# Kernel tuning notes

Hardware: AMD Instinct MI355X
Metric: run time of the kernel (lower is better)

The kernel has to match this reference:

```python
import jax, jax.numpy as jnp
import numpy as np

EMBED_DIM = 96
OUT_DIM = 192
HEADS = 2
HEAD_DIM = OUT_DIM // HEADS  # 96
STRIDE_Q = (1, 2, 2)
STRIDE_KV = (1, 8, 8)
SCALE = 1.0 / float(np.sqrt(HEAD_DIM))


def layer_norm(x, g, b, eps=1e-5):
    m = jnp.mean(x, -1, keepdims=True)
    v = jnp.mean(jnp.square(x - m), -1, keepdims=True)
    return (x - m) * jax.lax.rsqrt(v + eps) * g + b


def pool(x, thw, conv_w, g, b, stride):
    # x: [B, heads, N, d] with cls token at position 0; depthwise conv3d pool + LayerNorm(d)
    B, nh, N, d = x.shape
    T, H, W = thw
    cls_tok, rest = x[:, :, :1], x[:, :, 1:]
    rest = rest.transpose(0, 1, 3, 2).reshape(B * nh, d, T, H, W)
    rest = jax.lax.conv_general_dilated(
        rest, conv_w, stride, [(1, 1), (1, 1), (1, 1)],
        dimension_numbers=('NCDHW', 'OIDHW', 'NCDHW'), feature_group_count=d)
    T2, H2, W2 = rest.shape[2], rest.shape[3], rest.shape[4]
    rest = rest.reshape(B, nh, d, -1).transpose(0, 1, 3, 2)
    x = jnp.concatenate([cls_tok, rest], axis=2)
    return layer_norm(x, g, b), (T2, H2, W2)


def rel_idx(q_n, k_n):
    # decomposed relative-distance indices with q/k resolution ratio scaling
    q_r = max(k_n / q_n, 1.0)
    k_r = max(q_n / k_n, 1.0)
    d = (jnp.arange(q_n, dtype=jnp.float32)[:, None] * q_r
         - jnp.arange(k_n, dtype=jnp.float32)[None, :] * k_r + (k_n - 1) * k_r)
    return d.astype(jnp.int32)


def add_rel_pos(attn, q, q_thw, k_thw, rph, rpw, rpt):
    qt, qh, qw = q_thw
    kt, kh, kw = k_thw
    Rh = rph[rel_idx(qh, kh)]  # [qh, kh, d]
    Rw = rpw[rel_idx(qw, kw)]  # [qw, kw, d]
    Rt = rpt[rel_idx(qt, kt)]  # [qt, kt, d]
    B, nh, qN, d = q.shape
    r_q = q[:, :, 1:].reshape(B, nh, qt, qh, qw, d)
    rel_h = jnp.einsum('bythwc,hkc->bythwk', r_q, Rh)  # k = kh
    rel_w = jnp.einsum('bythwc,wkc->bythwk', r_q, Rw)  # k = kw
    rel_t = jnp.einsum('bythwc,tkc->bythwk', r_q, Rt)  # k = kt
    rel = (rel_t[..., :, None, None] + rel_h[..., None, :, None]
           + rel_w[..., None, None, :]).reshape(B, nh, qt * qh * qw, kt * kh * kw)
    return attn.at[:, :, 1:, 1:].add(rel)


def _forward(x, qkv_w, qkv_b, proj_w, proj_b, pq_w, nq_g, nq_b, pk_w, nk_g, nk_b,
             pv_w, nv_g, nv_b, rel_pos_h, rel_pos_w, rel_pos_t, thw):
    B, N, C = x.shape
    qkv = (x @ qkv_w.T + qkv_b).reshape(B, N, 3, HEADS, HEAD_DIM).transpose(2, 0, 3, 1, 4)
    q, k, v = qkv[0], qkv[1], qkv[2]  # each [B, heads, N, head_dim]
    k, k_thw = pool(k, thw, pk_w, nk_g, nk_b, STRIDE_KV)
    v, _ = pool(v, thw, pv_w, nv_g, nv_b, STRIDE_KV)
    q, q_thw = pool(q, thw, pq_w, nq_g, nq_b, STRIDE_Q)
    attn = jnp.einsum('bhqd,bhkd->bhqk', q * SCALE, k)
    attn = add_rel_pos(attn, q, q_thw, k_thw, rel_pos_h, rel_pos_w, rel_pos_t)
    attn = jax.nn.softmax(attn, axis=-1)
    out = jnp.einsum('bhqk,bhkd->bhqd', attn, v) + q  # residual_pool, with cls embed
    out = out.transpose(0, 2, 1, 3).reshape(B, -1, OUT_DIM)
    return out @ proj_w.T + proj_b


def setup_inputs() -> dict:
    key = jax.random.key(0)
    ks = jax.random.split(key, 10)
    T, H, W = 8, 56, 56
    N = 1 + T * H * W  # 25089
    B = 4
    std = 0.02
    return {
        'x': jax.random.normal(ks[0], (B, N, EMBED_DIM), jnp.float32),
        'qkv_w': jax.random.normal(ks[1], (3 * OUT_DIM, EMBED_DIM), jnp.float32) * std,
        'qkv_b': jnp.zeros((3 * OUT_DIM,), jnp.float32),
        'proj_w': jax.random.normal(ks[2], (OUT_DIM, OUT_DIM), jnp.float32) * std,
        'proj_b': jnp.zeros((OUT_DIM,), jnp.float32),
        'pq_w': jax.random.normal(ks[3], (HEAD_DIM, 1, 3, 3, 3), jnp.float32) * std,
        'nq_g': jnp.ones((HEAD_DIM,), jnp.float32),
        'nq_b': jnp.zeros((HEAD_DIM,), jnp.float32),
        'pk_w': jax.random.normal(ks[4], (HEAD_DIM, 1, 3, 3, 3), jnp.float32) * std,
        'nk_g': jnp.ones((HEAD_DIM,), jnp.float32),
        'nk_b': jnp.zeros((HEAD_DIM,), jnp.float32),
        'pv_w': jax.random.normal(ks[5], (HEAD_DIM, 1, 3, 3, 3), jnp.float32) * std,
        'nv_g': jnp.ones((HEAD_DIM,), jnp.float32),
        'nv_b': jnp.zeros((HEAD_DIM,), jnp.float32),
        'rel_pos_h': jax.random.normal(ks[6], (55, HEAD_DIM), jnp.float32) * std,
        'rel_pos_w': jax.random.normal(ks[7], (55, HEAD_DIM), jnp.float32) * std,
        'rel_pos_t': jax.random.normal(ks[8], (15, HEAD_DIM), jnp.float32) * std,
        'thw_t': 8, 'thw_h': 56, 'thw_w': 56,
    }


def reference(x, qkv_w, qkv_b, proj_w, proj_b, pq_w, nq_g, nq_b, pk_w, nk_g, nk_b,
              pv_w, nv_g, nv_b, rel_pos_h, rel_pos_w, rel_pos_t, thw_t, thw_h, thw_w):
    thw = (int(thw_t), int(thw_h), int(thw_w))
    return _forward(x, qkv_w, qkv_b, proj_w, proj_b, pq_w, nq_g, nq_b, pk_w, nk_g, nk_b,
                    pv_w, nv_g, nv_b, rel_pos_h, rel_pos_w, rel_pos_t, thw)
```

## Files before the change

kernel.cpp:

```cpp
#include <hip/hip_runtime.h>
#include <hip/hip_bf16.h>

typedef short short8 __attribute__((ext_vector_type(8)));
typedef float floatx4 __attribute__((ext_vector_type(4)));
typedef float floatx4v __attribute__((ext_vector_type(4)));

#define SCALE_F 0.10206207261596575f

static __device__ __forceinline__ float b2f(unsigned short u){
  unsigned int v = ((unsigned int)u) << 16; float f;
  __builtin_memcpy(&f, &v, 4); return f;
}
static __device__ __forceinline__ unsigned short f2b(float f){
  __hip_bfloat16 h = __float2bfloat16(f);
  unsigned short u; __builtin_memcpy(&u, &h, 2); return u;
}
static __device__ __forceinline__ int map20(int i){
  return (i < 2) ? i : 7 + ((i-2)/3)*8 + ((i-2)%3);
}

struct ConvDesc {
  const void* src[17];
  long long off[17];
  int count[17];
};

__global__ __launch_bounds__(256) void k_convert(ConvDesc d, unsigned short* dst_base,
                                                 int* flagp, const unsigned int* xprobe)
{
  __shared__ int sflag;
  if (threadIdx.x < 64){
    unsigned int w = xprobe[1024 + threadIdx.x];
    int e = (w >> 7) & 0xFF;
    int pl = (e >= 90 && e <= 140) ? 1 : 0;
    unsigned long long m = __ballot(pl);
    if (threadIdx.x == 0){
      sflag = (__popcll(m) < 40) ? 1 : 0;
      if (blockIdx.x == 0 && blockIdx.y == 0) *flagp = sflag;
    }
  }
  __syncthreads();
  const int flag = sflag;
  const int t = blockIdx.y + 1;
  const int cnt = d.count[t];
  unsigned short* dst = dst_base + d.off[t];
  const float* sf = (const float*)d.src[t];
  const unsigned short* su = (const unsigned short*)d.src[t];
  for (int i = blockIdx.x*blockDim.x + threadIdx.x; i < cnt; i += gridDim.x*blockDim.x){
    dst[i] = flag ? f2b(sf[i]) : su[i];
  }
}

static __device__ __forceinline__ void load_x_frag(
    const void* xr_, int flag, size_t elem_off, short8& a0, short8& a1, short8& a2)
{
  if (flag){
    const float* xr = (const float*)xr_ + elem_off;
    floatx4v f0 = *(const floatx4v*)(xr),      f1 = *(const floatx4v*)(xr+4);
    floatx4v f2 = *(const floatx4v*)(xr+32),   f3 = *(const floatx4v*)(xr+36);
    floatx4v f4 = *(const floatx4v*)(xr+64),   f5 = *(const floatx4v*)(xr+68);
    #pragma unroll
    for (int j = 0; j < 4; ++j){
      a0[j] = (short)f2b(f0[j]); a0[j+4] = (short)f2b(f1[j]);
      a1[j] = (short)f2b(f2[j]); a1[j+4] = (short)f2b(f3[j]);
      a2[j] = (short)f2b(f4[j]); a2[j+4] = (short)f2b(f5[j]);
    }
  } else {
    const unsigned short* xr = (const unsigned short*)xr_ + elem_off;
    a0 = *(const short8*)(xr);
    a1 = *(const short8*)(xr + 32);
    a2 = *(const short8*)(xr + 64);
  }
}

__global__ __launch_bounds__(256) void k_qkv_q(
    const void* __restrict__ x, const unsigned short* __restrict__ w,
    const unsigned short* __restrict__ bias, unsigned short* __restrict__ qr,
    const int* __restrict__ flagp)
{
  const int flag = *flagp;
  const int lane = threadIdx.x & 63;
  const int wv = threadIdx.x >> 6;
  const int kq = (lane >> 4) * 8;
  const int m_base = blockIdx.x * 64 + wv * 16;

  int ma = m_base + (lane & 15); if (ma > 100355) ma = 100355;
  short8 a0, a1, a2;
  load_x_frag(x, flag, (size_t)ma*96 + kq, a0, a1, a2);

  size_t base0[4];
  int mrow[4];
  #pragma unroll
  for (int r = 0; r < 4; ++r){
    int m = m_base + (lane >> 4)*4 + r;
    mrow[r] = m;
    int bb = m / 25089; int n = m - bb*25089;
    base0[r] = ((size_t)(bb*2)*25089 + n)*96;
  }

  #pragma unroll
  for (int ct = 0; ct < 12; ++ct){
    int col = ct*16 + (lane & 15);
    const unsigned short* wrow = w + col*96 + kq;
    short8 b0 = *(const short8*)(wrow);
    short8 b1 = *(const short8*)(wrow + 32);
    short8 b2 = *(const short8*)(wrow + 64);
    float bv = b2f(bias[col]);
    floatx4 acc = {0.f,0.f,0.f,0.f};
    acc = __builtin_amdgcn_mfma_f32_16x16x32_bf16(a0, b0, acc, 0,0,0);
    acc = __builtin_amdgcn_mfma_f32_16x16x32_bf16(a1, b1, acc, 0,0,0);
    acc = __builtin_amdgcn_mfma_f32_16x16x32_bf16(a2, b2, acc, 0,0,0);
    const int head = ct / 6;
    const int dstat = (ct % 6) * 16;
    size_t hoff = (size_t)head * 2408544 + dstat + (lane & 15);
    #pragma unroll
    for (int r = 0; r < 4; ++r){
      if (mrow[r] < 100356) qr[base0[r] + hoff] = f2b(acc[r] + bv);
    }
  }
}

__global__ __launch_bounds__(256) void k_qkv_kv(
    const void* __restrict__ x, const unsigned short* __restrict__ w,
    const unsigned short* __restrict__ bias,
    unsigned short* __restrict__ kc, unsigned short* __restrict__ vc,
    unsigned short* __restrict__ kcls, unsigned short* __restrict__ vcls,
    const int* __restrict__ flagp)
{
  const int flag = *flagp;
  const int isv = blockIdx.y;
  const int lane = threadIdx.x & 63;
  const int wv = threadIdx.x >> 6;
  const int kq = (lane >> 4) * 8;
  const int quad = lane >> 4;
  const int col_l = lane & 15;
  const int rbase = blockIdx.x * 64 + wv * 16;

  int rhoA = rbase + col_l; if (rhoA > 12803) rhoA = 12803;
  int bA, nA;
  if (rhoA < 4){ bA = rhoA; nA = 0; }
  else {
    int rp = rhoA - 4;
    bA = rp / 3200; int rem = rp - bA*3200;
    int t = rem / 400; int s = rem - t*400;
    int ry = s / 20, rx = s - ry*20;
    nA = 1 + (t*56 + map20(ry))*56 + map20(rx);
  }
  short8 a0, a1, a2;
  load_x_frag(x, flag, ((size_t)bA*25089 + nA)*96 + kq, a0, a1, a2);

  int isCls[4], bI[4], baseI[4], valid[4];
  #pragma unroll
  for (int r = 0; r < 4; ++r){
    int rho = rbase + quad*4 + r;
    valid[r] = (rho < 12804);
    if (rho > 12803) rho = 12803;
    if (rho < 4){ isCls[r] = 1; bI[r] = rho; baseI[r] = 0; }
    else {
      int rp = rho - 4;
      int b = rp / 3200; int rem = rp - b*3200;
      int t = rem / 400; int s = rem - t*400;
      int ry = s / 20, rx = s - ry*20;
      isCls[r] = 0; bI[r] = b;
      baseI[r] = (((b*8 + t)*20 + ry)*20 + rx)*192;
    }
  }

  unsigned short* buf  = isv ? vc : kc;
  unsigned short* bufc = isv ? vcls : kcls;
  #pragma unroll
  for (int ct = 0; ct < 12; ++ct){
    const int col = 192 + (isv*12 + ct)*16 + col_l;
    const unsigned short* wrow = w + col*96 + kq;
    short8 b0 = *(const short8*)(wrow);
    short8 b1 = *(const short8*)(wrow + 32);
    short8 b2 = *(const short8*)(wrow + 64);
    float bv = b2f(bias[col]);
    floatx4 acc = {0.f,0.f,0.f,0.f};
    acc = __builtin_amdgcn_mfma_f32_16x16x32_bf16(a0, b0, acc, 0,0,0);
    acc = __builtin_amdgcn_mfma_f32_16x16x32_bf16(a1, b1, acc, 0,0,0);
    acc = __builtin_amdgcn_mfma_f32_16x16x32_bf16(a2, b2, acc, 0,0,0);
    const int head = ct / 6;
    const int dstat = (ct % 6) * 16;
    #pragma unroll
    for (int r = 0; r < 4; ++r){
      if (valid[r]){
        float o = acc[r] + bv;
        if (isCls[r]) bufc[(bI[r]*2 + head)*96 + dstat + col_l] = f2b(o);
        else          buf[baseI[r] + head*96 + dstat + col_l]   = f2b(o);
      }
    }
  }
}

__global__ __launch_bounds__(384) void k_poolq(
    const unsigned short* __restrict__ qr, const unsigned short* __restrict__ cw,
    const unsigned short* __restrict__ g, const unsigned short* __restrict__ bta,
    unsigned short* __restrict__ qp)
{
  __shared__ float wlds[27*96];
  __shared__ float gls[96], bls[96];
  __shared__ float ls1[29*12], ls2[29*12];
  __shared__ float lmean[29], linvs[29];

  const int y  = blockIdx.x;
  const int t  = blockIdx.y;
  const int bh = blockIdx.z;
  const int tid = threadIdx.x;
  const bool has_cls = (y == 0 && t == 0);
  const unsigned short* base = qr + (size_t)bh*2408544;

  for (int idx = tid; idx < 27*96; idx += 384){
    int tap = idx / 96, d = idx - tap*96;
    wlds[idx] = b2f(cw[d*27 + tap]);
  }
  for (int idx = tid; idx < 96; idx += 384){
    gls[idx] = b2f(g[idx]); bls[idx] = b2f(bta[idx]);
  }
  __syncthreads();

  const int x = tid / 12, dg = tid - x*12;
  float val[8] = {0,0,0,0,0,0,0,0};

  if (x < 28){
    #pragma unroll
    for (int dt = 0; dt < 3; ++dt){
      int tt = t + dt - 1; if (tt < 0 || tt >= 8) continue;
      #pragma unroll
      for (int dy = 0; dy < 3; ++dy){
        int yy = 2*y + dy - 1; if (yy < 0 || yy >= 56) continue;
        #pragma unroll
        for (int dx = 0; dx < 3; ++dx){
          int xv = 2*x + dx - 1; if (xv < 0 || xv >= 56) continue;
          const int tap = (dt*3+dy)*3+dx;
          short8 v = *(const short8*)(base + (size_t)(1 + (tt*56 + yy)*56 + xv)*96 + dg*8);
          const float* wr = wlds + tap*96 + dg*8;
          #pragma unroll
          for (int j = 0; j < 8; ++j) val[j] += b2f((unsigned short)v[j]) * wr[j];
        }
      }
    }
    float s1 = 0.f, s2 = 0.f;
    #pragma unroll
    for (int j = 0; j < 8; ++j){ s1 += val[j]; s2 += val[j]*val[j]; }
    ls1[x*12+dg] = s1; ls2[x*12+dg] = s2;
  } else if (has_cls && tid >= 348 && tid < 360){
    int cdg = tid - 348;
    short8 v = *(const short8*)(base + cdg*8);
    float s1 = 0.f, s2 = 0.f;
    #pragma unroll
    for (int j = 0; j < 8; ++j){ val[j] = b2f((unsigned short)v[j]); s1 += val[j]; s2 += val[j]*val[j]; }
    ls1[28*12+cdg] = s1; ls2[28*12+cdg] = s2;
  }
  __syncthreads();

  if (tid < 28 || (tid == 28 && has_cls)){
    float s1 = 0.f, s2 = 0.f;
    #pragma unroll
    for (int k = 0; k < 12; ++k){ s1 += ls1[tid*12+k]; s2 += ls2[tid*12+k]; }
    float mean = s1 * (1.f/96.f);
    float var  = s2 * (1.f/96.f) - mean*mean;
    lmean[tid] = mean; linvs[tid] = rsqrtf(var + 1e-5f);
  }
  __syncthreads();

  if (x < 28){
    float mean = lmean[x], inv = linvs[x];
    int tok = 1 + (t*28 + y)*28 + x;
    short8 o;
    #pragma unroll
    for (int j = 0; j < 8; ++j)
      o[j] = (short)f2b((val[j] - mean)*inv*gls[dg*8+j] + bls[dg*8+j]);
    *(short8*)(qp + ((size_t)bh*6273 + tok)*96 + dg*8) = o;
  } else if (has_cls && tid >= 348 && tid < 360){
    int cdg = tid - 348;
    float mean = lmean[28], inv = linvs[28];
    short8 o;
    #pragma unroll
    for (int j = 0; j < 8; ++j)
      o[j] = (short)f2b((val[j] - mean)*inv*gls[cdg*8+j] + bls[cdg*8+j]);
    *(short8*)(qp + (size_t)bh*6273*96 + cdg*8) = o;
  }
}

__global__ __launch_bounds__(128) void k_poolkv(
    const unsigned short* __restrict__ kc, const unsigned short* __restrict__ vc,
    const unsigned short* __restrict__ kcls, const unsigned short* __restrict__ vcls,
    const unsigned short* __restrict__ cwk, const unsigned short* __restrict__ gk, const unsigned short* __restrict__ bk,
    const unsigned short* __restrict__ cwv, const unsigned short* __restrict__ gv, const unsigned short* __restrict__ bv,
    unsigned short* __restrict__ kp, unsigned short* __restrict__ vt)
{
  const int bid = blockIdx.x;
  const int isv = blockIdx.y;
  const int bh = bid / 416; const int key = bid - bh*416;
  const int d = threadIdx.x;
  if (key >= 393){
    if (d < 96){
      if (isv == 0) kp[((size_t)bh*416 + key)*96 + d] = 0;
      else          vt[((size_t)bh*96 + d)*416 + key] = 0;
    }
    return;
  }
  const int b = bh >> 1, head = bh & 1;
  const unsigned short* buf  = isv ? vc : kc;
  const unsigned short* bufc = isv ? vcls : kcls;
  const unsigned short* cw = (isv == 0) ? cwk : cwv;
  const unsigned short* g  = (isv == 0) ? gk : gv;
  const unsigned short* bt = (isv == 0) ? bk : bv;
  float val = 0.f;
  if (d < 96){
    if (key == 0) val = b2f(bufc[bh*96 + d]);
    else {
      int s = key - 1; int t = s / 49; int r2 = s - t*49; int y = r2 / 7; int xx = r2 - y*7;
      const unsigned short* wr = cw + d*27;
      float sum = 0.f;
      #pragma unroll
      for (int dt = 0; dt < 3; ++dt){
        int tt = t + dt - 1; if (tt < 0 || tt >= 8) continue;
        #pragma unroll
        for (int dy = 0; dy < 3; ++dy){
          if (y == 0 && dy == 0) continue;
          int ry = (y == 0) ? (dy - 1) : 2 + 3*(y-1) + dy;
          #pragma unroll
          for (int dx = 0; dx < 3; ++dx){
            if (xx == 0 && dx == 0) continue;
            int rx = (xx == 0) ? (dx - 1) : 2 + 3*(xx-1) + dx;
            sum += b2f(buf[(((b*8 + tt)*20 + ry)*20 + rx)*192 + head*96 + d]) * b2f(wr[(dt*3+dy)*3+dx]);
          }
        }
      }
      val = sum;
    }
  }
  __shared__ float r1[128], r2s[128];
  r1[threadIdx.x] = (d < 96) ? val : 0.f;
  r2s[threadIdx.x] = (d < 96) ? val*val : 0.f;
  __syncthreads();
  for (int off = 64; off > 0; off >>= 1){
    if ((int)threadIdx.x < off){ r1[threadIdx.x] += r1[threadIdx.x+off]; r2s[threadIdx.x] += r2s[threadIdx.x+off]; }
    __syncthreads();
  }
  if (d < 96){
    float mean = r1[0] * (1.f/96.f);
    float var  = r2s[0] * (1.f/96.f) - mean*mean;
    float inv = rsqrtf(var + 1e-5f);
    float o = (val - mean)*inv*b2f(g[d]) + b2f(bt[d]);
    if (isv == 0) kp[((size_t)bh*416 + key)*96 + d] = f2b(o);
    else          vt[((size_t)bh*96 + d)*416 + key] = f2b(o);
  }
}

__global__ __launch_bounds__(256) void k_rel(
    const unsigned short* __restrict__ qp,
    const unsigned short* __restrict__ rph, const unsigned short* __restrict__ rpw,
    const unsigned short* __restrict__ rpt,
    float* __restrict__ Trel)
{
  const int lane = threadIdx.x & 63;
  const int wv = threadIdx.x >> 6;
  const int bh = blockIdx.y;
  const int q0 = blockIdx.x*64 + wv*16;
  const int kq = (lane >> 4) * 8;
  const int quad = lane >> 4;
  const int col_l = lane & 15;

  const unsigned short* qbase = qp + (size_t)bh*6273*96;
  int qa = q0 + col_l; if (qa > 6272) qa = 6272;
  const unsigned short* qrow = qbase + (size_t)qa*96 + kq;
  short8 a0 = *(const short8*)(qrow);
  short8 a1 = *(const short8*)(qrow + 32);
  short8 a2 = *(const short8*)(qrow + 64);

  int yq[4], xq[4], tq[4], liv[4];
  #pragma unroll
  for (int r = 0; r < 4; ++r){
    int gq = q0 + quad*4 + r;
    liv[r] = (gq >= 1 && gq <= 6272);
    int s = (gq >= 1) ? gq - 1 : 0;
    tq[r] = s / 784; int r2 = s - tq[r]*784; yq[r] = r2 / 28; xq[r] = r2 - yq[r]*28;
  }
  float* Tb = Trel + (size_t)bh*6273*24;

  #pragma unroll
  for (int ct = 0; ct < 8; ++ct){
    int c = ct*16 + col_l;
    const unsigned short* rrow;
    if (c < 55)       rrow = rph + (size_t)c*96;
    else if (c < 110) rrow = rpw + (size_t)(c-55)*96;
    else { int ci = c-110; if (ci > 14) ci = 14; rrow = rpt + (size_t)ci*96; }
    rrow += kq;
    short8 b0 = *(const short8*)(rrow);
    short8 b1 = *(const short8*)(rrow + 32);
    short8 b2 = *(const short8*)(rrow + 64);
    floatx4 acc = {0.f,0.f,0.f,0.f};
    acc = __builtin_amdgcn_mfma_f32_16x16x32_bf16(a0, b0, acc, 0,0,0);
    acc = __builtin_amdgcn_mfma_f32_16x16x32_bf16(a1, b1, acc, 0,0,0);
    acc = __builtin_amdgcn_mfma_f32_16x16x32_bf16(a2, b2, acc, 0,0,0);
    #pragma unroll
    for (int r = 0; r < 4; ++r){
      int gq = q0 + quad*4 + r;
      if (!liv[r] || gq > 6272) continue;
      float* Tq = Tb + (size_t)gq*24;
      if (c < 55){
        int u = yq[r] + 24 - c;
        if (u >= 0 && u <= 24 && (u & 3) == 0) Tq[u >> 2] = acc[r];
      } else if (c < 110){
        int u = xq[r] + 24 - (c - 55);
        if (u >= 0 && u <= 24 && (u & 3) == 0) Tq[8 + (u >> 2)] = acc[r];
      } else if (c < 125){
        int u = tq[r] + 7 - (c - 110);
        if (u >= 0 && u <= 7) Tq[16 + u] = acc[r];
      }
    }
  }
}

#define PSTR 424
__global__ __launch_bounds__(128) void k_attn(
    const unsigned short* __restrict__ qp, const unsigned short* __restrict__ kp,
    const unsigned short* __restrict__ vt, const float* __restrict__ Trel,
    unsigned short* __restrict__ ao)
{
  __shared__ unsigned short P[2][16*PSTR];
  __shared__ float rel[2][16*24];

  const int bh = blockIdx.y;
  const int bb = bh >> 1, head = bh & 1;
  const int tid = threadIdx.x;
  const int lane = tid & 63;
  const int wv = tid >> 6;
  const int q0 = (blockIdx.x*2 + wv)*16;

  const unsigned short* qbase = qp + (size_t)bh*6273*96;
  const unsigned short* kbase = kp + (size_t)bh*416*96;
  const unsigned short* vbase = vt + (size_t)bh*96*416;

  float* relw = &rel[wv][0];
  #pragma unroll
  for (int it = 0; it < 2; ++it){
    int idx = lane + it*64;
    if (idx < 96){
      int row = idx / 6, seg = idx - row*6;
      int gq = q0 + row; if (gq > 6272) gq = 6272;
      *(floatx4v*)(relw + row*24 + seg*4) =
        *(const floatx4v*)(Trel + ((size_t)bh*6273 + gq)*24 + seg*4);
    }
  }

  const int col = lane & 15;
  const int quad = lane >> 4;
  const int kq = quad * 8;

  short8 a0, a1, a2;
  {
    int qa = q0 + col; if (qa > 6272) qa = 6272;
    const unsigned short* qrow = qbase + (size_t)qa*96 + kq;
    a0 = *(const short8*)(qrow);
    a1 = *(const short8*)(qrow + 32);
    a2 = *(const short8*)(qrow + 64);
  }

  int liv[4];
  const float* Tm[4];
  #pragma unroll
  for (int r = 0; r < 4; ++r){
    int gq = q0 + quad*4 + r;
    liv[r] = (gq >= 1);
    Tm[r] = relw + (quad*4 + r)*24;
  }

  floatx4 acc[25];
  float mx[4] = {-1e30f,-1e30f,-1e30f,-1e30f};
  #pragma unroll
  for (int t = 0; t < 25; ++t){
    const unsigned short* krow = kbase + (size_t)(t*16 + col)*96 + kq;
    short8 b0 = *(const short8*)(krow);
    short8 b1 = *(const short8*)(krow + 32);
    short8 b2 = *(const short8*)(krow + 64);
    floatx4 a = {0.f,0.f,0.f,0.f};
    a = __builtin_amdgcn_mfma_f32_16x16x32_bf16(a0, b0, a, 0,0,0);
    a = __builtin_amdgcn_mfma_f32_16x16x32_bf16(a1, b1, a, 0,0,0);
    a = __builtin_amdgcn_mfma_f32_16x16x32_bf16(a2, b2, a, 0,0,0);
    const int key = t*16 + col;
    const bool validk = (t < 24) || (col <= 8);
    int kt = 0, ky = 0, kx = 0;
    if (key >= 1){
      int ks = key - 1; kt = ks / 49; int krm = ks - kt*49; ky = krm / 7; kx = krm - ky*7;
    }
    #pragma unroll
    for (int r = 0; r < 4; ++r){
      float s;
      if (!validk) s = -1e30f;
      else {
        s = a[r] * SCALE_F;
        if (key >= 1 && liv[r])
          s += Tm[r][ky] + Tm[r][8 + kx] + Tm[r][16 + kt];
      }
      a[r] = s;
      mx[r] = fmaxf(mx[r], s);
    }
    acc[t] = a;
  }
  #pragma unroll
  for (int r = 0; r < 4; ++r){
    #pragma unroll
    for (int o = 1; o < 16; o <<= 1) mx[r] = fmaxf(mx[r], __shfl_xor(mx[r], o, 64));
  }
  float sum[4] = {0.f,0.f,0.f,0.f};
  #pragma unroll
  for (int t = 0; t < 25; ++t){
    #pragma unroll
    for (int r = 0; r < 4; ++r){
      float e = __expf(acc[t][r] - mx[r]);
      acc[t][r] = e; sum[r] += e;
    }
  }
  float linv4[4];
  #pragma unroll
  for (int r = 0; r < 4; ++r){
    #pragma unroll
    for (int o = 1; o < 16; o <<= 1) sum[r] += __shfl_xor(sum[r], o, 64);
    linv4[r] = 1.f / sum[r];
  }

  unsigned short* Pw = &P[wv][0];
  #pragma unroll
  for (int t = 0; t < 25; ++t){
    #pragma unroll
    for (int r = 0; r < 4; ++r)
      Pw[(quad*4 + r)*PSTR + t*16 + col] = f2b(acc[t][r]);
  }
  #pragma unroll
  for (int r = 0; r < 4; ++r)
    Pw[(quad*4 + r)*PSTR + 400 + col] = 0;

  short8 pf[13];
  #pragma unroll
  for (int s = 0; s < 13; ++s)
    pf[s] = *(const short8*)(Pw + col*PSTR + s*32 + kq);

  #pragma unroll
  for (int dt = 0; dt < 6; ++dt){
    const int dd = dt*16 + col;
    const unsigned short* vrow = vbase + (size_t)dd*416 + kq;
    floatx4 o = {0.f,0.f,0.f,0.f};
    #pragma unroll
    for (int s = 0; s < 13; ++s){
      short8 vf = *(const short8*)(vrow + s*32);
      o = __builtin_amdgcn_mfma_f32_16x16x32_bf16(pf[s], vf, o, 0,0,0);
    }
    #pragma unroll
    for (int r = 0; r < 4; ++r){
      int gq = q0 + quad*4 + r;
      if (gq <= 6272){
        float val = o[r] * linv4[r] + b2f(qbase[(size_t)gq*96 + dd]);
        ao[((size_t)bb*6273 + gq)*192 + head*96 + dd] = f2b(val);
      }
    }
  }
}

__global__ __launch_bounds__(256) void k_proj(
    const unsigned short* __restrict__ ao, const unsigned short* __restrict__ w,
    const unsigned short* __restrict__ bias, void* __restrict__ out, const int* __restrict__ flagp)
{
  const int flag = *flagp;
  const int lane = threadIdx.x & 63;
  const int wv = threadIdx.x >> 6;
  const int c = blockIdx.y*64 + wv*16 + (lane & 15);
  const int kq = (lane >> 4) * 8;
  short8 bfr[6];
  const unsigned short* wrow = w + c*192 + kq;
  #pragma unroll
  for (int s = 0; s < 6; ++s) bfr[s] = *(const short8*)(wrow + 32*s);
  float bv = b2f(bias[c]);
  const int m_base = blockIdx.x * 64;
  for (int i = 0; i < 4; ++i){
    int mt = m_base + i*16;
    int ma = mt + (lane & 15); if (ma > 25091) ma = 25091;
    const unsigned short* arow = ao + (size_t)ma*192 + kq;
    floatx4 acc = {0.f,0.f,0.f,0.f};
    #pragma unroll
    for (int s = 0; s < 6; ++s){
      short8 a = *(const short8*)(arow + 32*s);
      acc = __builtin_amdgcn_mfma_f32_16x16x32_bf16(a, bfr[s], acc, 0,0,0);
    }
    #pragma unroll
    for (int r = 0; r < 4; ++r){
      int m = mt + (lane >> 4)*4 + r;
      if (m < 25092){
        float o = acc[r] + bv;
        if (flag) ((float*)out)[(size_t)m*192 + c] = o;
        else      ((unsigned short*)out)[(size_t)m*192 + c] = f2b(o);
      }
    }
  }
}

extern "C" void kernel_launch(void* const* d_in, const int* in_sizes, int n_in,
                              void* d_out, int out_size, void* d_ws, size_t ws_size,
                              hipStream_t stream)
{
  char* p = (char*)d_ws;
  int* flagp = (int*)p; p += 16;
  unsigned short* conv = (unsigned short*)p;

  ConvDesc desc;
  long long cum = 0;
  for (int i = 0; i < 17; ++i){
    desc.src[i] = d_in[i];
    desc.off[i] = cum;
    desc.count[i] = in_sizes[i];
    cum += in_sizes[i];
  }
  p += (size_t)cum * 2;

  unsigned short* q_raw  = (unsigned short*)p; p += (size_t)19268352*2;
  unsigned short* kc     = (unsigned short*)p; p += (size_t)2457600*2;
  unsigned short* vc     = (unsigned short*)p; p += (size_t)2457600*2;
  unsigned short* kcls   = (unsigned short*)p; p += (size_t)768*2;
  unsigned short* vcls   = (unsigned short*)p; p += (size_t)768*2;
  unsigned short* q_pool = (unsigned short*)p; p += (size_t)4817664*2;
  unsigned short* k_pool = (unsigned short*)p; p += (size_t)319488*2;
  unsigned short* v_t    = (unsigned short*)p; p += (size_t)319488*2;
  float*          Trel   = (float*)p;         p += (size_t)8*6273*24*4;
  unsigned short* a_out  = q_raw;

  const unsigned short* cqkv_w = conv + desc.off[1];
  const unsigned short* cqkv_b = conv + desc.off[2];
  const unsigned short* cproj_w= conv + desc.off[3];
  const unsigned short* cproj_b= conv + desc.off[4];
  const unsigned short* cpq_w  = conv + desc.off[5];
  const unsigned short* cnq_g  = conv + desc.off[6];
  const unsigned short* cnq_b  = conv + desc.off[7];
  const unsigned short* cpk_w  = conv + desc.off[8];
  const unsigned short* cnk_g  = conv + desc.off[9];
  const unsigned short* cnk_b  = conv + desc.off[10];
  const unsigned short* cpv_w  = conv + desc.off[11];
  const unsigned short* cnv_g  = conv + desc.off[12];
  const unsigned short* cnv_b  = conv + desc.off[13];
  const unsigned short* crph   = conv + desc.off[14];
  const unsigned short* crpw   = conv + desc.off[15];
  const unsigned short* crpt   = conv + desc.off[16];

  k_convert<<<dim3(16, 16), 256, 0, stream>>>(desc, conv, flagp, (const unsigned int*)d_in[0]);
  k_qkv_q <<<dim3(1569), 256, 0, stream>>>(d_in[0], cqkv_w, cqkv_b, q_raw, flagp);
  k_qkv_kv<<<dim3(201, 2), 256, 0, stream>>>(d_in[0], cqkv_w, cqkv_b, kc, vc, kcls, vcls, flagp);
  k_poolq<<<dim3(28, 8, 8), 384, 0, stream>>>(q_raw, cpq_w, cnq_g, cnq_b, q_pool);
  k_poolkv<<<dim3(8*416, 2), 128, 0, stream>>>(kc, vc, kcls, vcls, cpk_w, cnk_g, cnk_b, cpv_w, cnv_g, cnv_b, k_pool, v_t);
  k_rel  <<<dim3(99, 8), 256, 0, stream>>>(q_pool, crph, crpw, crpt, Trel);
  k_attn <<<dim3(197, 8), 128, 0, stream>>>(q_pool, k_pool, v_t, Trel, a_out);
  k_proj <<<dim3(393, 3), 256, 0, stream>>>(a_out, cproj_w, cproj_b, d_out, flagp);
}
```

Measured before the change: 306.0 us.

## Split attention key range across two waves per 16-query tile

Each block now handles one 16-query tile, and its two waves split the key tiles (13 and 12) instead of each wave owning its own query tile. Partial row maxima and sums are merged through shared memory with block barriers. The two waves then split the output head dimension for the PV product, reading the shared P buffer. This doubles the grid and halves the per-wave score accumulators, which eases register pressure and should raise occupancy. The cost is two __syncthreads per block and each wave loading the full P and V ranges for its half of the output.

```diff
diff --git a/kernel.cpp b/kernel.cpp
--- a/kernel.cpp
+++ b/kernel.cpp
@@ -421,28 +421,28 @@
     const unsigned short* __restrict__ vt, const float* __restrict__ Trel,
     unsigned short* __restrict__ ao)
 {
-  __shared__ unsigned short P[2][16*PSTR];
-  __shared__ float rel[2][16*24];
+  __shared__ unsigned short P[16*PSTR];
+  __shared__ float rel[16*24];
+  __shared__ float mx_sh[2][16], sum_sh[2][16];
 
   const int bh = blockIdx.y;
   const int bb = bh >> 1, head = bh & 1;
   const int tid = threadIdx.x;
   const int lane = tid & 63;
   const int wv = tid >> 6;
-  const int q0 = (blockIdx.x*2 + wv)*16;
+  const int q0 = blockIdx.x * 16;
 
   const unsigned short* qbase = qp + (size_t)bh*6273*96;
   const unsigned short* kbase = kp + (size_t)bh*416*96;
   const unsigned short* vbase = vt + (size_t)bh*96*416;
 
-  float* relw = &rel[wv][0];
   #pragma unroll
   for (int it = 0; it < 2; ++it){
     int idx = lane + it*64;
     if (idx < 96){
       int row = idx / 6, seg = idx - row*6;
       int gq = q0 + row; if (gq > 6272) gq = 6272;
-      *(floatx4v*)(relw + row*24 + seg*4) =
+      *(floatx4v*)(rel + row*24 + seg*4) =
         *(const floatx4v*)(Trel + ((size_t)bh*6273 + gq)*24 + seg*4);
     }
   }
@@ -450,6 +450,8 @@
   const int col = lane & 15;
   const int quad = lane >> 4;
   const int kq = quad * 8;
+  const int t0 = wv ? 13 : 0;
+  const int NT = wv ? 12 : 13;
 
   short8 a0, a1, a2;
   {
@@ -466,13 +468,15 @@
   for (int r = 0; r < 4; ++r){
     int gq = q0 + quad*4 + r;
     liv[r] = (gq >= 1);
-    Tm[r] = relw + (quad*4 + r)*24;
-  }
-
-  floatx4 acc[25];
+    Tm[r] = rel + (quad*4 + r)*24;
+  }
+
+  floatx4 acc[13];
   float mx[4] = {-1e30f,-1e30f,-1e30f,-1e30f};
   #pragma unroll
-  for (int t = 0; t < 25; ++t){
+  for (int i = 0; i < 13; ++i){
+    if (i >= NT) break;
+    const int t = t0 + i;
     const unsigned short* krow = kbase + (size_t)(t*16 + col)*96 + kq;
     short8 b0 = *(const short8*)(krow);
     short8 b1 = *(const short8*)(krow + 32);
@@ -482,7 +486,7 @@
     a = __builtin_amdgcn_mfma_f32_16x16x32_bf16(a1, b1, a, 0,0,0);
     a = __builtin_amdgcn_mfma_f32_16x16x32_bf16(a2, b2, a, 0,0,0);
     const int key = t*16 + col;
-    const bool validk = (t < 24) || (col <= 8);
+    const bool validk = (key < 393);
     int kt = 0, ky = 0, kx = 0;
     if (key >= 1){
       int ks = key - 1; kt = ks / 49; int krm = ks - kt*49; ky = krm / 7; kx = krm - ky*7;
@@ -499,49 +503,70 @@
       a[r] = s;
       mx[r] = fmaxf(mx[r], s);
     }
-    acc[t] = a;
+    acc[i] = a;
   }
   #pragma unroll
   for (int r = 0; r < 4; ++r){
     #pragma unroll
     for (int o = 1; o < 16; o <<= 1) mx[r] = fmaxf(mx[r], __shfl_xor(mx[r], o, 64));
   }
+  if (col == 0){
+    #pragma unroll
+    for (int r = 0; r < 4; ++r) mx_sh[wv][quad*4 + r] = mx[r];
+  }
+  __syncthreads();
+
+  float M[4];
+  #pragma unroll
+  for (int r = 0; r < 4; ++r)
+    M[r] = fmaxf(mx_sh[0][quad*4 + r], mx_sh[1][quad*4 + r]);
   float sum[4] = {0.f,0.f,0.f,0.f};
   #pragma unroll
-  for (int t = 0; t < 25; ++t){
+  for (int i = 0; i < 13; ++i){
+    if (i >= NT) break;
     #pragma unroll
     for (int r = 0; r < 4; ++r){
-      float e = __expf(acc[t][r] - mx[r]);
-      acc[t][r] = e; sum[r] += e;
-    }
-  }
+      float e = __expf(acc[i][r] - M[r]);
+      acc[i][r] = e; sum[r] += e;
+    }
+  }
+  #pragma unroll
+  for (int r = 0; r < 4; ++r){
+    #pragma unroll
+    for (int o = 1; o < 16; o <<= 1) sum[r] += __shfl_xor(sum[r], o, 64);
+  }
+  if (col == 0){
+    #pragma unroll
+    for (int r = 0; r < 4; ++r) sum_sh[wv][quad*4 + r] = sum[r];
+  }
+  #pragma unroll
+  for (int i = 0; i < 13; ++i){
+    if (i >= NT) break;
+    const int t = t0 + i;
+    #pragma unroll
+    for (int r = 0; r < 4; ++r)
+      P[(quad*4 + r)*PSTR + t*16 + col] = f2b(acc[i][r]);
+  }
+  if (wv == 1){
+    #pragma unroll
+    for (int r = 0; r < 4; ++r)
+      P[(quad*4 + r)*PSTR + 400 + col] = 0;
+  }
+  __syncthreads();
+
   float linv4[4];
   #pragma unroll
-  for (int r = 0; r < 4; ++r){
-    #pragma unroll
-    for (int o = 1; o < 16; o <<= 1) sum[r] += __shfl_xor(sum[r], o, 64);
-    linv4[r] = 1.f / sum[r];
-  }
-
-  unsigned short* Pw = &P[wv][0];
-  #pragma unroll
-  for (int t = 0; t < 25; ++t){
-    #pragma unroll
-    for (int r = 0; r < 4; ++r)
-      Pw[(quad*4 + r)*PSTR + t*16 + col] = f2b(acc[t][r]);
-  }
-  #pragma unroll
   for (int r = 0; r < 4; ++r)
-    Pw[(quad*4 + r)*PSTR + 400 + col] = 0;
+    linv4[r] = 1.f / (sum_sh[0][quad*4 + r] + sum_sh[1][quad*4 + r]);
 
   short8 pf[13];
   #pragma unroll
   for (int s = 0; s < 13; ++s)
-    pf[s] = *(const short8*)(Pw + col*PSTR + s*32 + kq);
-
-  #pragma unroll
-  for (int dt = 0; dt < 6; ++dt){
-    const int dd = dt*16 + col;
+    pf[s] = *(const short8*)(P + col*PSTR + s*32 + kq);
+
+  #pragma unroll
+  for (int dti = 0; dti < 3; ++dti){
+    const int dd = (wv*3 + dti)*16 + col;
     const unsigned short* vrow = vbase + (size_t)dd*416 + kq;
     floatx4 o = {0.f,0.f,0.f,0.f};
     #pragma unroll
@@ -649,6 +674,6 @@
   k_poolq<<<dim3(28, 8, 8), 384, 0, stream>>>(q_raw, cpq_w, cnq_g, cnq_b, q_pool);
   k_poolkv<<<dim3(8*416, 2), 128, 0, stream>>>(kc, vc, kcls, vcls, cpk_w, cnk_g, cnk_b, cpv_w, cnv_g, cnv_b, k_pool, v_t);
   k_rel  <<<dim3(99, 8), 256, 0, stream>>>(q_pool, crph, crpw, crpt, Trel);
-  k_attn <<<dim3(197, 8), 128, 0, stream>>>(q_pool, k_pool, v_t, Trel, a_out);
+  k_attn <<<dim3(393, 8), 128, 0, stream>>>(q_pool, k_pool, v_t, Trel, a_out);
   k_proj <<<dim3(393, 3), 256, 0, stream>>>(a_out, cproj_w, cproj_b, d_out, flagp);
 }
```

Measured after the change: 329.6 us. 1.08x slower.
